# Performance work log

Measured on AMD Instinct MI355X. Metric: run time of the kernel, lower is better.

The kernel has to match this reference:

```python
import jax, jax.numpy as jnp
import numpy as np

B, N, M, D = 32, 1024, 256, 512
NEG_INF = -1e9  # keras Softmax mask additive constant


def _length_mask(key, batch, length):
    # realistic padding masks: first L positions valid, L >= length//4
    lens = jax.random.randint(key, (batch,), length // 4, length + 1)
    return jnp.arange(length)[None, :] < lens[:, None]


def setup_inputs() -> dict:
    key = jax.random.key(0)
    k1, k2, k3, k4, k5 = jax.random.split(key, 5)
    context = jax.random.normal(k1, (B, N, D), dtype=jnp.float32)
    query = jax.random.normal(k2, (B, M, D), dtype=jnp.float32)
    c_mask = _length_mask(k3, B, N)
    q_mask = _length_mask(k4, B, M)
    # Dense(units=1, use_bias=False) kernel over concat([q, c, q*c]) -> (3D, 1)
    w = jax.random.normal(k5, (3 * D, 1), dtype=jnp.float32) * (1.0 / np.sqrt(3 * D))
    return {"context": context, "query": query, "c_mask": c_mask, "q_mask": q_mask, "w": w}


def reference(context, query, c_mask, q_mask, w):
    d = context.shape[-1]
    # stack order in original: [q_matrix, c_matrix, q*c]
    w_q = w[:d, 0]
    w_c = w[d:2 * d, 0]
    w_m = w[2 * d:, 0]
    # trilinear similarity S[b,n,m] = q_j.w_q + c_i.w_c + (c_i*q_j).w_m, decomposed
    S = (context @ w_c)[:, :, None] \
        + (query @ w_q)[:, None, :] \
        + jnp.einsum('bnd,bmd->bnm', context * w_m, query)
    # context-direction softmax over query axis (axis=2), masked by q_mask
    A = jax.nn.softmax(jnp.where(q_mask[:, None, :], S, NEG_INF), axis=2)
    # query-direction softmax over context axis (axis=1), masked by c_mask
    Bm = jax.nn.softmax(jnp.where(c_mask[:, :, None], S, NEG_INF), axis=1)
    # context-to-query attention: A @ query -> (b, n, d)
    c2q = jnp.einsum('bnm,bmd->bnd', A, query)
    # query-to-context: (A @ B^T) @ context -> (b, n, d)
    q2c = jnp.einsum('bnk,bjk,bjd->bnd', A, Bm, context)
    out = jnp.concatenate([context, c2q, context * c2q, context * q2c], axis=-1)
    return out
```

## Files before the change

### kernel.cpp

```cpp
#include <hip/hip_runtime.h>
#include <hip/hip_bf16.h>

#define B_ 32
#define N_ 1024
#define M_ 256
#define D_ 512

typedef __attribute__((ext_vector_type(8))) short short8;
typedef __attribute__((ext_vector_type(4))) float f32x4;

#define OFF_S     ((size_t)0)
#define OFF_CTXW  ((size_t)8388608)
#define OFF_ANM   ((size_t)8388608)
#define OFF_BMT   ((size_t)12582912)
#define OFF_QB    ((size_t)16777216)
#define OFF_QT    ((size_t)18874368)
#define OFF_CT    ((size_t)20971520)
#define OFF_CDOT  ((size_t)29360128)
#define OFF_QDOT  ((size_t)29392896)
#define OFF_RMAX  ((size_t)29401088)
#define OFF_RSUM  ((size_t)29433856)
#define OFF_CMAX  ((size_t)29466624)
#define OFF_CSUM  ((size_t)29474816)
#define OFF_PMAX  ((size_t)29483008)
#define OFF_PSUM  ((size_t)29614080)


__global__ __launch_bounds__(256) void prep_ctxw(
    const float* __restrict__ ctx, const float* __restrict__ w,
    __hip_bfloat16* __restrict__ ctxw)
{
    size_t i4 = ((size_t)blockIdx.x * 256 + threadIdx.x) * 4;
    int d = (int)(i4 & (D_ - 1));
    float4 c = *(const float4*)(ctx + i4);
    float4 wm = *(const float4*)(w + 2 * D_ + d);
    __hip_bfloat16 o[4] __attribute__((aligned(8)));
    o[0] = __float2bfloat16(c.x * wm.x);
    o[1] = __float2bfloat16(c.y * wm.y);
    o[2] = __float2bfloat16(c.z * wm.z);
    o[3] = __float2bfloat16(c.w * wm.w);
    *(ushort4*)(ctxw + i4) = *(ushort4*)o;
}

__global__ __launch_bounds__(256) void prep_qry(
    const float* __restrict__ qry, __hip_bfloat16* __restrict__ qb)
{
    size_t i4 = ((size_t)blockIdx.x * 256 + threadIdx.x) * 4;
    float4 c = *(const float4*)(qry + i4);
    __hip_bfloat16 o[4] __attribute__((aligned(8)));
    o[0] = __float2bfloat16(c.x);
    o[1] = __float2bfloat16(c.y);
    o[2] = __float2bfloat16(c.z);
    o[3] = __float2bfloat16(c.w);
    *(ushort4*)(qb + i4) = *(ushort4*)o;
}

__global__ __launch_bounds__(256) void transpose_cast(
    const float* __restrict__ src, __hip_bfloat16* __restrict__ dst,
    int rows, int cols)
{
    __shared__ float t[64][65];
    int b = blockIdx.z, r0 = blockIdx.y * 64, c0 = blockIdx.x * 64;
    int tr = threadIdx.x >> 6, tc = threadIdx.x & 63;
    const float* sp = src + ((size_t)b * rows + r0) * cols + c0;
#pragma unroll
    for (int i = 0; i < 16; ++i)
        t[tr + i * 4][tc] = sp[(size_t)(tr + i * 4) * cols + tc];
    __syncthreads();
    __hip_bfloat16* dp = dst + ((size_t)b * cols + c0) * rows + r0;
#pragma unroll
    for (int i = 0; i < 16; ++i)
        dp[(size_t)(tr + i * 4) * rows + tc] = __float2bfloat16(t[tc][tr + i * 4]);
}

__global__ __launch_bounds__(256) void dots_kernel(
    const float* __restrict__ ctx, const float* __restrict__ qry,
    const float* __restrict__ w, float* __restrict__ cdot, float* __restrict__ qdot)
{
    int row  = blockIdx.x * 4 + (threadIdx.x >> 6);
    int lane = threadIdx.x & 63;
    const float* src; const float* wp; float* dst;
    if (row < B_ * N_) {
        src = ctx + (size_t)row * D_; wp = w + D_;
        dst = cdot + row;
    } else {
        int rr = row - B_ * N_;
        src = qry + (size_t)rr * D_; wp = w;
        dst = qdot + rr;
    }
    float s = 0.f;
#pragma unroll
    for (int i = 0; i < D_ / 64; ++i)
        s = fmaf(src[lane + 64 * i], wp[lane + 64 * i], s);
#pragma unroll
    for (int off = 32; off; off >>= 1) s += __shfl_down(s, off, 64);
    if (lane == 0) *dst = s;
}


__device__ __forceinline__ void gl2lds16(const __hip_bfloat16* g, __hip_bfloat16* l) {
    __builtin_amdgcn_global_load_lds(
        (const __attribute__((address_space(1))) unsigned int*)g,
        (__attribute__((address_space(3))) unsigned int*)l, 16, 0, 0);
}

template<int KTOT>
__device__ __forceinline__ void mfma128(
    const __hip_bfloat16* __restrict__ Abase, int lda,
    const __hip_bfloat16* __restrict__ Bbase, int ldb,
    __hip_bfloat16* As, __hip_bfloat16* Bs, f32x4 acc[4][4])
{
    const int tid = threadIdx.x;
    const int w = tid >> 6, lane = tid & 63;
    const int quad = lane >> 4, lr = lane & 15;
    const int wr = w >> 1, wc = w & 1;
    const int srow = w * 32 + (lane >> 2);
    const int scol = (lane & 3) * 8;
    const __hip_bfloat16* ga0 = Abase + (size_t)srow * lda + scol;
    const __hip_bfloat16* ga1 = ga0 + (size_t)16 * lda;
    const __hip_bfloat16* gb0 = Bbase + (size_t)srow * ldb + scol;
    const __hip_bfloat16* gb1 = gb0 + (size_t)16 * ldb;
    __hip_bfloat16* la0 = As + w * 1024;
    __hip_bfloat16* la1 = As + w * 1024 + 512;
    __hip_bfloat16* lb0 = Bs + w * 1024;
    __hip_bfloat16* lb1 = Bs + w * 1024 + 512;
    const int aoff = (wr * 64 + lr) * 32 + quad * 8;
    const int boff = (wc * 64 + lr) * 32 + quad * 8;

    for (int k0 = 0; k0 < KTOT; k0 += 32) {
        gl2lds16(ga0, la0); gl2lds16(ga1, la1);
        gl2lds16(gb0, lb0); gl2lds16(gb1, lb1);
        ga0 += 32; ga1 += 32; gb0 += 32; gb1 += 32;
        asm volatile("s_waitcnt vmcnt(0)" ::: "memory");
        __syncthreads();
        short8 a[4], bb[4];
        const short8* ap = (const short8*)(As + aoff);
        const short8* bp = (const short8*)(Bs + boff);
#pragma unroll
        for (int fi = 0; fi < 4; ++fi) a[fi] = ap[fi * 64];
#pragma unroll
        for (int fj = 0; fj < 4; ++fj) bb[fj] = bp[fj * 64];
#pragma unroll
        for (int fi = 0; fi < 4; ++fi)
#pragma unroll
            for (int fj = 0; fj < 4; ++fj)
                acc[fi][fj] = __builtin_amdgcn_mfma_f32_16x16x32_bf16(
                    a[fi], bb[fj], acc[fi][fj], 0, 0, 0);
        __syncthreads();
    }
}

#define ACC_INIT f32x4 acc[4][4]; \
    _Pragma("unroll") for (int i = 0; i < 4; ++i) \
    _Pragma("unroll") for (int j = 0; j < 4; ++j) acc[i][j] = (f32x4){0.f, 0.f, 0.f, 0.f};

#define EPI_IDX const int tid = threadIdx.x, lane = tid & 63, quad = lane >> 4, lr = lane & 15; \
    const int wr = tid >> 7, wc = (tid >> 6) & 1;

__global__ __launch_bounds__(256) void s_gemm_mfma(
    const __hip_bfloat16* __restrict__ ctxw, const __hip_bfloat16* __restrict__ qryb,
    const float* __restrict__ cdot, const float* __restrict__ qdot,
    float* __restrict__ S)
{
    __shared__ __align__(16) __hip_bfloat16 As[4096], Bs[4096];
    const int b = blockIdx.z, n0 = blockIdx.y * 128, m0 = blockIdx.x * 128;
    ACC_INIT
    mfma128<512>(ctxw + ((size_t)b * N_ + n0) * D_, D_,
                 qryb + ((size_t)b * M_ + m0) * D_, D_, As, Bs, acc);
    EPI_IDX
#pragma unroll
    for (int fi = 0; fi < 4; ++fi) {
#pragma unroll
        for (int r = 0; r < 4; ++r) {
            int n = n0 + wr * 64 + fi * 16 + quad * 4 + r;
            float cd = cdot[b * N_ + n];
            size_t rowoff = ((size_t)b * N_ + n) * M_;
#pragma unroll
            for (int fj = 0; fj < 4; ++fj) {
                int m = m0 + wc * 64 + fj * 16 + lr;
                S[rowoff + m] = acc[fi][fj][r] + cd + qdot[b * M_ + m];
            }
        }
    }
}

__global__ __launch_bounds__(256) void q2cpart_mfma(
    const __hip_bfloat16* __restrict__ ctxT, const __hip_bfloat16* __restrict__ BmT,
    __hip_bfloat16* __restrict__ Q2CT)
{
    __shared__ __align__(16) __hip_bfloat16 As[4096], Bs[4096];
    const int b = blockIdx.z, d0 = blockIdx.y * 128, m0 = blockIdx.x * 128;
    ACC_INIT
    mfma128<1024>(ctxT + ((size_t)b * D_ + d0) * N_, N_,
                  BmT + ((size_t)b * M_ + m0) * N_, N_, As, Bs, acc);
    EPI_IDX
#pragma unroll
    for (int fi = 0; fi < 4; ++fi) {
#pragma unroll
        for (int r = 0; r < 4; ++r) {
            int d = d0 + wr * 64 + fi * 16 + quad * 4 + r;
#pragma unroll
            for (int fj = 0; fj < 4; ++fj) {
                int m = m0 + wc * 64 + fj * 16 + lr;
                Q2CT[((size_t)b * D_ + d) * M_ + m] = __float2bfloat16(acc[fi][fj][r]);
            }
        }
    }
}

__global__ __launch_bounds__(256) void c2q_mfma(
    const __hip_bfloat16* __restrict__ Anm, const __hip_bfloat16* __restrict__ qryT,
    const float* __restrict__ ctx, float* __restrict__ out)
{
    __shared__ __align__(16) __hip_bfloat16 As[4096], Bs[4096];
    const int b = blockIdx.z, n0 = blockIdx.y * 128, d0 = blockIdx.x * 128;
    ACC_INIT
    mfma128<256>(Anm + ((size_t)b * N_ + n0) * M_, M_,
                 qryT + ((size_t)b * D_ + d0) * M_, M_, As, Bs, acc);
    EPI_IDX
#pragma unroll
    for (int fi = 0; fi < 4; ++fi) {
#pragma unroll
        for (int r = 0; r < 4; ++r) {
            int n = n0 + wr * 64 + fi * 16 + quad * 4 + r;
            size_t ibase = ((size_t)b * N_ + n) * D_;
            size_t obase = ((size_t)b * N_ + n) * (4 * D_);
#pragma unroll
            for (int fj = 0; fj < 4; ++fj) {
                int d = d0 + wc * 64 + fj * 16 + lr;
                float c = ctx[ibase + d];
                float v = acc[fi][fj][r];
                out[obase + d] = c;
                out[obase + D_ + d] = v;
                out[obase + 2 * D_ + d] = c * v;
            }
        }
    }
}

__global__ __launch_bounds__(256) void q2c_mfma(
    const __hip_bfloat16* __restrict__ Anm, const __hip_bfloat16* __restrict__ Q2CT,
    const float* __restrict__ ctx, float* __restrict__ out)
{
    __shared__ __align__(16) __hip_bfloat16 As[4096], Bs[4096];
    const int b = blockIdx.z, n0 = blockIdx.y * 128, d0 = blockIdx.x * 128;
    ACC_INIT
    mfma128<256>(Anm + ((size_t)b * N_ + n0) * M_, M_,
                 Q2CT + ((size_t)b * D_ + d0) * M_, M_, As, Bs, acc);
    EPI_IDX
#pragma unroll
    for (int fi = 0; fi < 4; ++fi) {
#pragma unroll
        for (int r = 0; r < 4; ++r) {
            int n = n0 + wr * 64 + fi * 16 + quad * 4 + r;
            size_t ibase = ((size_t)b * N_ + n) * D_;
            size_t obase = ((size_t)b * N_ + n) * (4 * D_);
#pragma unroll
            for (int fj = 0; fj < 4; ++fj) {
                int d = d0 + wc * 64 + fj * 16 + lr;
                out[obase + 3 * D_ + d] = ctx[ibase + d] * acc[fi][fj][r];
            }
        }
    }
}


__global__ __launch_bounds__(256) void row_stats(
    const float* __restrict__ S, const int* __restrict__ q_mask,
    float* __restrict__ rmax, float* __restrict__ rsum)
{
    int row  = blockIdx.x * 4 + (threadIdx.x >> 6);
    int lane = threadIdx.x & 63;
    int b = row >> 10;
    const float* Sp = S + (size_t)row * M_;
    const int* qm = q_mask + b * M_;
    float v[4];
    float mx = -1e30f;
#pragma unroll
    for (int i = 0; i < 4; ++i) {
        int m = lane + 64 * i;
        float x = qm[m] ? Sp[m] : -1e9f;
        v[i] = x; mx = fmaxf(mx, x);
    }
#pragma unroll
    for (int off = 32; off; off >>= 1) mx = fmaxf(mx, __shfl_down(mx, off, 64));
    mx = __shfl(mx, 0, 64);
    float sm = 0.f;
#pragma unroll
    for (int i = 0; i < 4; ++i) sm += __expf(v[i] - mx);
#pragma unroll
    for (int off = 32; off; off >>= 1) sm += __shfl_down(sm, off, 64);
    if (lane == 0) { rmax[row] = mx; rsum[row] = sm; }
}

__global__ __launch_bounds__(256) void col_stats_part(
    const float* __restrict__ S, const int* __restrict__ c_mask,
    float* __restrict__ pmax, float* __restrict__ psum)
{
    int b = blockIdx.y, ch = blockIdx.x, m = threadIdx.x;
    const float* Sp = S + ((size_t)b * N_ + ch * 64) * M_;
    const int* cm = c_mask + b * N_ + ch * 64;
    float mx = -1e30f, sm = 0.f;
    for (int n = 0; n < 64; ++n) {
        float x = cm[n] ? Sp[(size_t)n * M_ + m] : -1e9f;
        if (x > mx) { sm = sm * __expf(mx - x) + 1.f; mx = x; }
        else        { sm += __expf(x - mx); }
    }
    pmax[((size_t)b * 16 + ch) * M_ + m] = mx;
    psum[((size_t)b * 16 + ch) * M_ + m] = sm;
}

__global__ __launch_bounds__(256) void col_stats_combine(
    const float* __restrict__ pmax, const float* __restrict__ psum,
    float* __restrict__ cmax, float* __restrict__ csum)
{
    int idx = blockIdx.x * 256 + threadIdx.x;
    int b = idx >> 8, m = idx & 255;
    float mx = -1e30f;
#pragma unroll
    for (int ch = 0; ch < 16; ++ch)
        mx = fmaxf(mx, pmax[((size_t)b * 16 + ch) * M_ + m]);
    float sm = 0.f;
#pragma unroll
    for (int ch = 0; ch < 16; ++ch)
        sm += psum[((size_t)b * 16 + ch) * M_ + m] *
              __expf(pmax[((size_t)b * 16 + ch) * M_ + m] - mx);
    cmax[idx] = mx; csum[idx] = sm;
}

__global__ __launch_bounds__(256) void normalize_kernel(
    const float* __restrict__ S, __hip_bfloat16* __restrict__ Anm,
    __hip_bfloat16* __restrict__ BmT,
    const int* __restrict__ q_mask, const int* __restrict__ c_mask,
    const float* __restrict__ rmax, const float* __restrict__ rsum,
    const float* __restrict__ cmax, const float* __restrict__ csum)
{
    __shared__ float t[64][65];
    int b = blockIdx.z, n0 = blockIdx.y * 64, m0 = blockIdx.x * 64;
    int tr = threadIdx.x >> 6, tc = threadIdx.x & 63;
    int m = m0 + tc;
    int qm = q_mask[b * M_ + m];
    float cmx = cmax[b * M_ + m], csm = csum[b * M_ + m];
#pragma unroll
    for (int i = 0; i < 16; ++i) {
        int n = n0 + tr + i * 4;
        size_t idx = ((size_t)b * N_ + n) * M_ + m;
        float s = S[idx];
        float a  = qm ? __expf(s - rmax[b * N_ + n]) / rsum[b * N_ + n] : 0.f;
        float bm = c_mask[b * N_ + n] ? __expf(s - cmx) / csm : 0.f;
        Anm[idx] = __float2bfloat16(a);
        t[tc][tr + i * 4] = bm;
    }
    __syncthreads();
#pragma unroll
    for (int i = 0; i < 16; ++i) {
        int ml = tr + i * 4;
        BmT[((size_t)b * M_ + m0 + ml) * N_ + n0 + tc] = __float2bfloat16(t[ml][tc]);
    }
}

extern "C" void kernel_launch(void* const* d_in, const int* in_sizes, int n_in,
                              void* d_out, int out_size, void* d_ws, size_t ws_size,
                              hipStream_t stream) {
    const float* ctx   = (const float*)d_in[0];
    const float* qry   = (const float*)d_in[1];
    const int*   cmask = (const int*)d_in[2];
    const int*   qmask = (const int*)d_in[3];
    const float* w     = (const float*)d_in[4];
    float* out = (float*)d_out;
    float* ws  = (float*)d_ws;

    float* S = ws + OFF_S;
    __hip_bfloat16* ctxw = (__hip_bfloat16*)(ws + OFF_CTXW);
    __hip_bfloat16* Anm  = (__hip_bfloat16*)(ws + OFF_ANM);
    __hip_bfloat16* BmT  = (__hip_bfloat16*)(ws + OFF_BMT);
    __hip_bfloat16* qb   = (__hip_bfloat16*)(ws + OFF_QB);
    __hip_bfloat16* Q2CT = (__hip_bfloat16*)(ws + OFF_QB);
    __hip_bfloat16* qT   = (__hip_bfloat16*)(ws + OFF_QT);
    __hip_bfloat16* cT   = (__hip_bfloat16*)(ws + OFF_CT);
    float* cdot = ws + OFF_CDOT;
    float* qdot = ws + OFF_QDOT;
    float* rmax = ws + OFF_RMAX;
    float* rsum = ws + OFF_RSUM;
    float* cmx  = ws + OFF_CMAX;
    float* csm  = ws + OFF_CSUM;
    float* pmax = ws + OFF_PMAX;
    float* psum = ws + OFF_PSUM;

    prep_ctxw<<<B_ * N_ * D_ / 1024, 256, 0, stream>>>(ctx, w, ctxw);
    prep_qry<<<B_ * M_ * D_ / 1024, 256, 0, stream>>>(qry, qb);
    dim3 gtc(D_ / 64, N_ / 64, B_);
    transpose_cast<<<gtc, 256, 0, stream>>>(ctx, cT, N_, D_);
    dim3 gtq(D_ / 64, M_ / 64, B_);
    transpose_cast<<<gtq, 256, 0, stream>>>(qry, qT, M_, D_);
    dots_kernel<<<(B_ * N_ + B_ * M_) / 4, 256, 0, stream>>>(ctx, qry, w, cdot, qdot);

    dim3 gS(M_ / 128, N_ / 128, B_);
    s_gemm_mfma<<<gS, 256, 0, stream>>>(ctxw, qb, cdot, qdot, S);

    row_stats<<<B_ * N_ / 4, 256, 0, stream>>>(S, qmask, rmax, rsum);
    dim3 gC(16, B_);
    col_stats_part<<<gC, 256, 0, stream>>>(S, cmask, pmax, psum);
    col_stats_combine<<<B_ * M_ / 256, 256, 0, stream>>>(pmax, psum, cmx, csm);

    dim3 gN(M_ / 64, N_ / 64, B_);
    normalize_kernel<<<gN, 256, 0, stream>>>(S, Anm, BmT, qmask, cmask,
                                             rmax, rsum, cmx, csm);

    dim3 gP(M_ / 128, D_ / 128, B_);
    q2cpart_mfma<<<gP, 256, 0, stream>>>(cT, BmT, Q2CT);

    dim3 gO(D_ / 128, N_ / 128, B_);
    c2q_mfma<<<gO, 256, 0, stream>>>(Anm, qT, ctx, out);
    q2c_mfma<<<gO, 256, 0, stream>>>(Anm, Q2CT, ctx, out);
}
```

Measured before the change: 534.6 us.

## Fuse prep, softmax stats into S GEMM epilogue, and merge output GEMMs

Merges the cast, transpose and dot-product prep kernels into one pass per input, with atomics accumulating the dot products into a zeroed buffer. Computes per-tile row and column softmax partial max/sum inside the S GEMM epilogue, so row_stats and col_stats_part no longer re-read S, and a single kernel combines the partials. Fuses the c2q and q2c GEMMs into one kernel that shares the A tile loads and writes all four output slices. The cost is more launch-free atomics, higher register and LDS pressure in the fused kernels, and a small extra memset.

```diff
diff --git a/kernel.cpp b/kernel.cpp
--- a/kernel.cpp
+++ b/kernel.cpp
@@ -24,77 +24,66 @@
 #define OFF_CSUM  ((size_t)29474816)
 #define OFF_PMAX  ((size_t)29483008)
 #define OFF_PSUM  ((size_t)29614080)
-
-
-__global__ __launch_bounds__(256) void prep_ctxw(
+#define OFF_RPMAX ((size_t)29745152)
+#define OFF_RPSUM ((size_t)29876224)
+
+__global__ __launch_bounds__(256) void prep_ctx(
     const float* __restrict__ ctx, const float* __restrict__ w,
-    __hip_bfloat16* __restrict__ ctxw)
-{
-    size_t i4 = ((size_t)blockIdx.x * 256 + threadIdx.x) * 4;
-    int d = (int)(i4 & (D_ - 1));
-    float4 c = *(const float4*)(ctx + i4);
-    float4 wm = *(const float4*)(w + 2 * D_ + d);
-    __hip_bfloat16 o[4] __attribute__((aligned(8)));
-    o[0] = __float2bfloat16(c.x * wm.x);
-    o[1] = __float2bfloat16(c.y * wm.y);
-    o[2] = __float2bfloat16(c.z * wm.z);
-    o[3] = __float2bfloat16(c.w * wm.w);
-    *(ushort4*)(ctxw + i4) = *(ushort4*)o;
-}
-
-__global__ __launch_bounds__(256) void prep_qry(
-    const float* __restrict__ qry, __hip_bfloat16* __restrict__ qb)
-{
-    size_t i4 = ((size_t)blockIdx.x * 256 + threadIdx.x) * 4;
-    float4 c = *(const float4*)(qry + i4);
-    __hip_bfloat16 o[4] __attribute__((aligned(8)));
-    o[0] = __float2bfloat16(c.x);
-    o[1] = __float2bfloat16(c.y);
-    o[2] = __float2bfloat16(c.z);
-    o[3] = __float2bfloat16(c.w);
-    *(ushort4*)(qb + i4) = *(ushort4*)o;
-}
-
-__global__ __launch_bounds__(256) void transpose_cast(
-    const float* __restrict__ src, __hip_bfloat16* __restrict__ dst,
-    int rows, int cols)
+    __hip_bfloat16* __restrict__ ctxw, __hip_bfloat16* __restrict__ cT,
+    float* __restrict__ cdot)
 {
     __shared__ float t[64][65];
-    int b = blockIdx.z, r0 = blockIdx.y * 64, c0 = blockIdx.x * 64;
+    int b = blockIdx.z, n0 = blockIdx.y * 64, d0 = blockIdx.x * 64;
     int tr = threadIdx.x >> 6, tc = threadIdx.x & 63;
-    const float* sp = src + ((size_t)b * rows + r0) * cols + c0;
+    const float* sp = ctx + ((size_t)b * N_ + n0) * D_ + d0;
+    __hip_bfloat16* cwp = ctxw + ((size_t)b * N_ + n0) * D_ + d0;
+    float wmv = w[2 * D_ + d0 + tc];
+    float wcv = w[D_ + d0 + tc];
+#pragma unroll
+    for (int i = 0; i < 16; ++i) {
+        int r = tr + i * 4;
+        float x = sp[(size_t)r * D_ + tc];
+        t[r][tc] = x;
+        cwp[(size_t)r * D_ + tc] = __float2bfloat16(x * wmv);
+        float p = x * wcv;
+#pragma unroll
+        for (int off = 32; off; off >>= 1) p += __shfl_down(p, off, 64);
+        if (tc == 0) atomicAdd(cdot + b * N_ + n0 + r, p);
+    }
+    __syncthreads();
+    __hip_bfloat16* dp = cT + ((size_t)b * D_ + d0) * N_ + n0;
 #pragma unroll
     for (int i = 0; i < 16; ++i)
-        t[tr + i * 4][tc] = sp[(size_t)(tr + i * 4) * cols + tc];
+        dp[(size_t)(tr + i * 4) * N_ + tc] = __float2bfloat16(t[tc][tr + i * 4]);
+}
+
+__global__ __launch_bounds__(256) void prep_q(
+    const float* __restrict__ qry, const float* __restrict__ w,
+    __hip_bfloat16* __restrict__ qb, __hip_bfloat16* __restrict__ qT,
+    float* __restrict__ qdot)
+{
+    __shared__ float t[64][65];
+    int b = blockIdx.z, m0 = blockIdx.y * 64, d0 = blockIdx.x * 64;
+    int tr = threadIdx.x >> 6, tc = threadIdx.x & 63;
+    const float* sp = qry + ((size_t)b * M_ + m0) * D_ + d0;
+    __hip_bfloat16* qbp = qb + ((size_t)b * M_ + m0) * D_ + d0;
+    float wqv = w[d0 + tc];
+#pragma unroll
+    for (int i = 0; i < 16; ++i) {
+        int r = tr + i * 4;
+        float x = sp[(size_t)r * D_ + tc];
+        t[r][tc] = x;
+        qbp[(size_t)r * D_ + tc] = __float2bfloat16(x);
+        float p = x * wqv;
+#pragma unroll
+        for (int off = 32; off; off >>= 1) p += __shfl_down(p, off, 64);
+        if (tc == 0) atomicAdd(qdot + b * M_ + m0 + r, p);
+    }
     __syncthreads();
-    __hip_bfloat16* dp = dst + ((size_t)b * cols + c0) * rows + r0;
+    __hip_bfloat16* dp = qT + ((size_t)b * D_ + d0) * M_ + m0;
 #pragma unroll
     for (int i = 0; i < 16; ++i)
-        dp[(size_t)(tr + i * 4) * rows + tc] = __float2bfloat16(t[tc][tr + i * 4]);
-}
-
-__global__ __launch_bounds__(256) void dots_kernel(
-    const float* __restrict__ ctx, const float* __restrict__ qry,
-    const float* __restrict__ w, float* __restrict__ cdot, float* __restrict__ qdot)
-{
-    int row  = blockIdx.x * 4 + (threadIdx.x >> 6);
-    int lane = threadIdx.x & 63;
-    const float* src; const float* wp; float* dst;
-    if (row < B_ * N_) {
-        src = ctx + (size_t)row * D_; wp = w + D_;
-        dst = cdot + row;
-    } else {
-        int rr = row - B_ * N_;
-        src = qry + (size_t)rr * D_; wp = w;
-        dst = qdot + rr;
-    }
-    float s = 0.f;
-#pragma unroll
-    for (int i = 0; i < D_ / 64; ++i)
-        s = fmaf(src[lane + 64 * i], wp[lane + 64 * i], s);
-#pragma unroll
-    for (int off = 32; off; off >>= 1) s += __shfl_down(s, off, 64);
-    if (lane == 0) *dst = s;
+        dp[(size_t)(tr + i * 4) * M_ + tc] = __float2bfloat16(t[tc][tr + i * 4]);
 }
 
 
@@ -150,36 +139,166 @@
     }
 }
 
-#define ACC_INIT f32x4 acc[4][4]; \
-    _Pragma("unroll") for (int i = 0; i < 4; ++i) \
-    _Pragma("unroll") for (int j = 0; j < 4; ++j) acc[i][j] = (f32x4){0.f, 0.f, 0.f, 0.f};
+template<int KTOT>
+__device__ __forceinline__ void mfma128x2(
+    const __hip_bfloat16* __restrict__ Abase, int lda,
+    const __hip_bfloat16* __restrict__ B1base,
+    const __hip_bfloat16* __restrict__ B2base, int ldb,
+    __hip_bfloat16* As, __hip_bfloat16* B1s, __hip_bfloat16* B2s,
+    f32x4 acc1[4][4], f32x4 acc2[4][4])
+{
+    const int tid = threadIdx.x;
+    const int w = tid >> 6, lane = tid & 63;
+    const int quad = lane >> 4, lr = lane & 15;
+    const int wr = w >> 1, wc = w & 1;
+    const int srow = w * 32 + (lane >> 2);
+    const int scol = (lane & 3) * 8;
+    const __hip_bfloat16* ga0 = Abase + (size_t)srow * lda + scol;
+    const __hip_bfloat16* ga1 = ga0 + (size_t)16 * lda;
+    const __hip_bfloat16* gb10 = B1base + (size_t)srow * ldb + scol;
+    const __hip_bfloat16* gb11 = gb10 + (size_t)16 * ldb;
+    const __hip_bfloat16* gb20 = B2base + (size_t)srow * ldb + scol;
+    const __hip_bfloat16* gb21 = gb20 + (size_t)16 * ldb;
+    __hip_bfloat16* la0 = As + w * 1024;
+    __hip_bfloat16* la1 = la0 + 512;
+    __hip_bfloat16* lb10 = B1s + w * 1024;
+    __hip_bfloat16* lb11 = lb10 + 512;
+    __hip_bfloat16* lb20 = B2s + w * 1024;
+    __hip_bfloat16* lb21 = lb20 + 512;
+    const int aoff = (wr * 64 + lr) * 32 + quad * 8;
+    const int boff = (wc * 64 + lr) * 32 + quad * 8;
+
+    for (int k0 = 0; k0 < KTOT; k0 += 32) {
+        gl2lds16(ga0, la0); gl2lds16(ga1, la1);
+        gl2lds16(gb10, lb10); gl2lds16(gb11, lb11);
+        gl2lds16(gb20, lb20); gl2lds16(gb21, lb21);
+        ga0 += 32; ga1 += 32; gb10 += 32; gb11 += 32; gb20 += 32; gb21 += 32;
+        asm volatile("s_waitcnt vmcnt(0)" ::: "memory");
+        __syncthreads();
+        short8 a[4], b1[4], b2[4];
+        const short8* ap = (const short8*)(As + aoff);
+        const short8* bp1 = (const short8*)(B1s + boff);
+        const short8* bp2 = (const short8*)(B2s + boff);
+#pragma unroll
+        for (int fi = 0; fi < 4; ++fi) a[fi] = ap[fi * 64];
+#pragma unroll
+        for (int fj = 0; fj < 4; ++fj) { b1[fj] = bp1[fj * 64]; b2[fj] = bp2[fj * 64]; }
+#pragma unroll
+        for (int fi = 0; fi < 4; ++fi)
+#pragma unroll
+            for (int fj = 0; fj < 4; ++fj) {
+                acc1[fi][fj] = __builtin_amdgcn_mfma_f32_16x16x32_bf16(
+                    a[fi], b1[fj], acc1[fi][fj], 0, 0, 0);
+                acc2[fi][fj] = __builtin_amdgcn_mfma_f32_16x16x32_bf16(
+                    a[fi], b2[fj], acc2[fi][fj], 0, 0, 0);
+            }
+        __syncthreads();
+    }
+}
+
+#define ACC_INIT(acc) \
+    _Pragma("unroll") for (int i_ = 0; i_ < 4; ++i_) \
+    _Pragma("unroll") for (int j_ = 0; j_ < 4; ++j_) acc[i_][j_] = (f32x4){0.f, 0.f, 0.f, 0.f};
 
 #define EPI_IDX const int tid = threadIdx.x, lane = tid & 63, quad = lane >> 4, lr = lane & 15; \
     const int wr = tid >> 7, wc = (tid >> 6) & 1;
 
-__global__ __launch_bounds__(256) void s_gemm_mfma(
+__global__ __launch_bounds__(256) void s_gemm_stats(
     const __hip_bfloat16* __restrict__ ctxw, const __hip_bfloat16* __restrict__ qryb,
     const float* __restrict__ cdot, const float* __restrict__ qdot,
-    float* __restrict__ S)
+    const int* __restrict__ q_mask, const int* __restrict__ c_mask,
+    float* __restrict__ S,
+    float* __restrict__ rpmax, float* __restrict__ rpsum,
+    float* __restrict__ pmax, float* __restrict__ psum)
 {
     __shared__ __align__(16) __hip_bfloat16 As[4096], Bs[4096];
     const int b = blockIdx.z, n0 = blockIdx.y * 128, m0 = blockIdx.x * 128;
-    ACC_INIT
+    f32x4 acc[4][4];
+    ACC_INIT(acc)
     mfma128<512>(ctxw + ((size_t)b * N_ + n0) * D_, D_,
                  qryb + ((size_t)b * M_ + m0) * D_, D_, As, Bs, acc);
     EPI_IDX
-#pragma unroll
-    for (int fi = 0; fi < 4; ++fi) {
+    float cd[4][4]; int cmv[4][4];
+#pragma unroll
+    for (int fi = 0; fi < 4; ++fi)
 #pragma unroll
         for (int r = 0; r < 4; ++r) {
             int n = n0 + wr * 64 + fi * 16 + quad * 4 + r;
-            float cd = cdot[b * N_ + n];
+            cd[fi][r] = cdot[b * N_ + n];
+            cmv[fi][r] = c_mask[b * N_ + n];
+        }
+    float qd[4]; int qmv[4];
+#pragma unroll
+    for (int fj = 0; fj < 4; ++fj) {
+        int m = m0 + wc * 64 + fj * 16 + lr;
+        qd[fj] = qdot[b * M_ + m];
+        qmv[fj] = q_mask[b * M_ + m];
+    }
+#pragma unroll
+    for (int fi = 0; fi < 4; ++fi)
+#pragma unroll
+        for (int r = 0; r < 4; ++r) {
+            int n = n0 + wr * 64 + fi * 16 + quad * 4 + r;
             size_t rowoff = ((size_t)b * N_ + n) * M_;
 #pragma unroll
             for (int fj = 0; fj < 4; ++fj) {
                 int m = m0 + wc * 64 + fj * 16 + lr;
-                S[rowoff + m] = acc[fi][fj][r] + cd + qdot[b * M_ + m];
-            }
+                S[rowoff + m] = acc[fi][fj][r] + cd[fi][r] + qd[fj];
+            }
+        }
+    const int part = blockIdx.x * 2 + wc;
+#pragma unroll
+    for (int fi = 0; fi < 4; ++fi)
+#pragma unroll
+        for (int r = 0; r < 4; ++r) {
+            float xs[4], mx = -1e30f;
+#pragma unroll
+            for (int fj = 0; fj < 4; ++fj) {
+                xs[fj] = qmv[fj] ? (acc[fi][fj][r] + cd[fi][r] + qd[fj]) : -1e9f;
+                mx = fmaxf(mx, xs[fj]);
+            }
+#pragma unroll
+            for (int off = 1; off < 16; off <<= 1)
+                mx = fmaxf(mx, __shfl_xor(mx, off, 64));
+            float se = 0.f;
+#pragma unroll
+            for (int fj = 0; fj < 4; ++fj) se += __expf(xs[fj] - mx);
+#pragma unroll
+            for (int off = 1; off < 16; off <<= 1)
+                se += __shfl_xor(se, off, 64);
+            if (lr == 0) {
+                int n = n0 + wr * 64 + fi * 16 + quad * 4 + r;
+                rpmax[((size_t)b * N_ + n) * 4 + part] = mx;
+                rpsum[((size_t)b * N_ + n) * 4 + part] = se;
+            }
+        }
+    const int ch = blockIdx.y * 2 + wr;
+#pragma unroll
+    for (int fj = 0; fj < 4; ++fj) {
+        float mx = -1e30f;
+#pragma unroll
+        for (int fi = 0; fi < 4; ++fi)
+#pragma unroll
+            for (int r = 0; r < 4; ++r) {
+                float x = cmv[fi][r] ? (acc[fi][fj][r] + cd[fi][r] + qd[fj]) : -1e9f;
+                mx = fmaxf(mx, x);
+            }
+        mx = fmaxf(mx, __shfl_xor(mx, 16, 64));
+        mx = fmaxf(mx, __shfl_xor(mx, 32, 64));
+        float se = 0.f;
+#pragma unroll
+        for (int fi = 0; fi < 4; ++fi)
+#pragma unroll
+            for (int r = 0; r < 4; ++r) {
+                float x = cmv[fi][r] ? (acc[fi][fj][r] + cd[fi][r] + qd[fj]) : -1e9f;
+                se += __expf(x - mx);
+            }
+        se += __shfl_xor(se, 16, 64);
+        se += __shfl_xor(se, 32, 64);
+        if (lane < 16) {
+            int m = m0 + wc * 64 + fj * 16 + lr;
+            pmax[((size_t)b * 16 + ch) * M_ + m] = mx;
+            psum[((size_t)b * 16 + ch) * M_ + m] = se;
         }
     }
 }
@@ -190,7 +309,8 @@
 {
     __shared__ __align__(16) __hip_bfloat16 As[4096], Bs[4096];
     const int b = blockIdx.z, d0 = blockIdx.y * 128, m0 = blockIdx.x * 128;
-    ACC_INIT
+    f32x4 acc[4][4];
+    ACC_INIT(acc)
     mfma128<1024>(ctxT + ((size_t)b * D_ + d0) * N_, N_,
                   BmT + ((size_t)b * M_ + m0) * N_, N_, As, Bs, acc);
     EPI_IDX
@@ -208,15 +328,20 @@
     }
 }
 
-__global__ __launch_bounds__(256) void c2q_mfma(
+__global__ __launch_bounds__(256) void out_fused_mfma(
     const __hip_bfloat16* __restrict__ Anm, const __hip_bfloat16* __restrict__ qryT,
-    const float* __restrict__ ctx, float* __restrict__ out)
-{
-    __shared__ __align__(16) __hip_bfloat16 As[4096], Bs[4096];
+    const __hip_bfloat16* __restrict__ Q2CT, const float* __restrict__ ctx,
+    float* __restrict__ out)
+{
+    __shared__ __align__(16) __hip_bfloat16 As[4096], B1s[4096], B2s[4096];
     const int b = blockIdx.z, n0 = blockIdx.y * 128, d0 = blockIdx.x * 128;
-    ACC_INIT
-    mfma128<256>(Anm + ((size_t)b * N_ + n0) * M_, M_,
-                 qryT + ((size_t)b * D_ + d0) * M_, M_, As, Bs, acc);
+    f32x4 acc1[4][4], acc2[4][4];
+    ACC_INIT(acc1)
+    ACC_INIT(acc2)
+    mfma128x2<256>(Anm + ((size_t)b * N_ + n0) * M_, M_,
+                   qryT + ((size_t)b * D_ + d0) * M_,
+                   Q2CT + ((size_t)b * D_ + d0) * M_, M_,
+                   As, B1s, B2s, acc1, acc2);
     EPI_IDX
 #pragma unroll
     for (int fi = 0; fi < 4; ++fi) {
@@ -229,103 +354,50 @@
             for (int fj = 0; fj < 4; ++fj) {
                 int d = d0 + wc * 64 + fj * 16 + lr;
                 float c = ctx[ibase + d];
-                float v = acc[fi][fj][r];
+                float v1 = acc1[fi][fj][r];
+                float v2 = acc2[fi][fj][r];
                 out[obase + d] = c;
-                out[obase + D_ + d] = v;
-                out[obase + 2 * D_ + d] = c * v;
-            }
-        }
-    }
-}
-
-__global__ __launch_bounds__(256) void q2c_mfma(
-    const __hip_bfloat16* __restrict__ Anm, const __hip_bfloat16* __restrict__ Q2CT,
-    const float* __restrict__ ctx, float* __restrict__ out)
-{
-    __shared__ __align__(16) __hip_bfloat16 As[4096], Bs[4096];
-    const int b = blockIdx.z, n0 = blockIdx.y * 128, d0 = blockIdx.x * 128;
-    ACC_INIT
-    mfma128<256>(Anm + ((size_t)b * N_ + n0) * M_, M_,
-                 Q2CT + ((size_t)b * D_ + d0) * M_, M_, As, Bs, acc);
-    EPI_IDX
-#pragma unroll
-    for (int fi = 0; fi < 4; ++fi) {
-#pragma unroll
-        for (int r = 0; r < 4; ++r) {
-            int n = n0 + wr * 64 + fi * 16 + quad * 4 + r;
-            size_t ibase = ((size_t)b * N_ + n) * D_;
-            size_t obase = ((size_t)b * N_ + n) * (4 * D_);
-#pragma unroll
-            for (int fj = 0; fj < 4; ++fj) {
-                int d = d0 + wc * 64 + fj * 16 + lr;
-                out[obase + 3 * D_ + d] = ctx[ibase + d] * acc[fi][fj][r];
-            }
-        }
-    }
-}
-
-
-__global__ __launch_bounds__(256) void row_stats(
-    const float* __restrict__ S, const int* __restrict__ q_mask,
+                out[obase + D_ + d] = v1;
+                out[obase + 2 * D_ + d] = c * v1;
+                out[obase + 3 * D_ + d] = c * v2;
+            }
+        }
+    }
+}
+
+
+__global__ __launch_bounds__(256) void combine_stats(
+    const float* __restrict__ pmax, const float* __restrict__ psum,
+    const float* __restrict__ rpmax, const float* __restrict__ rpsum,
+    float* __restrict__ cmax, float* __restrict__ csum,
     float* __restrict__ rmax, float* __restrict__ rsum)
 {
-    int row  = blockIdx.x * 4 + (threadIdx.x >> 6);
-    int lane = threadIdx.x & 63;
-    int b = row >> 10;
-    const float* Sp = S + (size_t)row * M_;
-    const int* qm = q_mask + b * M_;
-    float v[4];
-    float mx = -1e30f;
-#pragma unroll
-    for (int i = 0; i < 4; ++i) {
-        int m = lane + 64 * i;
-        float x = qm[m] ? Sp[m] : -1e9f;
-        v[i] = x; mx = fmaxf(mx, x);
-    }
-#pragma unroll
-    for (int off = 32; off; off >>= 1) mx = fmaxf(mx, __shfl_down(mx, off, 64));
-    mx = __shfl(mx, 0, 64);
-    float sm = 0.f;
-#pragma unroll
-    for (int i = 0; i < 4; ++i) sm += __expf(v[i] - mx);
-#pragma unroll
-    for (int off = 32; off; off >>= 1) sm += __shfl_down(sm, off, 64);
-    if (lane == 0) { rmax[row] = mx; rsum[row] = sm; }
-}
-
-__global__ __launch_bounds__(256) void col_stats_part(
-    const float* __restrict__ S, const int* __restrict__ c_mask,
-    float* __restrict__ pmax, float* __restrict__ psum)
-{
-    int b = blockIdx.y, ch = blockIdx.x, m = threadIdx.x;
-    const float* Sp = S + ((size_t)b * N_ + ch * 64) * M_;
-    const int* cm = c_mask + b * N_ + ch * 64;
-    float mx = -1e30f, sm = 0.f;
-    for (int n = 0; n < 64; ++n) {
-        float x = cm[n] ? Sp[(size_t)n * M_ + m] : -1e9f;
-        if (x > mx) { sm = sm * __expf(mx - x) + 1.f; mx = x; }
-        else        { sm += __expf(x - mx); }
-    }
-    pmax[((size_t)b * 16 + ch) * M_ + m] = mx;
-    psum[((size_t)b * 16 + ch) * M_ + m] = sm;
-}
-
-__global__ __launch_bounds__(256) void col_stats_combine(
-    const float* __restrict__ pmax, const float* __restrict__ psum,
-    float* __restrict__ cmax, float* __restrict__ csum)
-{
     int idx = blockIdx.x * 256 + threadIdx.x;
-    int b = idx >> 8, m = idx & 255;
-    float mx = -1e30f;
-#pragma unroll
-    for (int ch = 0; ch < 16; ++ch)
-        mx = fmaxf(mx, pmax[((size_t)b * 16 + ch) * M_ + m]);
-    float sm = 0.f;
-#pragma unroll
-    for (int ch = 0; ch < 16; ++ch)
-        sm += psum[((size_t)b * 16 + ch) * M_ + m] *
-              __expf(pmax[((size_t)b * 16 + ch) * M_ + m] - mx);
-    cmax[idx] = mx; csum[idx] = sm;
+    if (idx < B_ * M_) {
+        int b = idx >> 8, m = idx & 255;
+        float mx = -1e30f;
+#pragma unroll
+        for (int ch = 0; ch < 16; ++ch)
+            mx = fmaxf(mx, pmax[((size_t)b * 16 + ch) * M_ + m]);
+        float sm = 0.f;
+#pragma unroll
+        for (int ch = 0; ch < 16; ++ch)
+            sm += psum[((size_t)b * 16 + ch) * M_ + m] *
+                  __expf(pmax[((size_t)b * 16 + ch) * M_ + m] - mx);
+        cmax[idx] = mx; csum[idx] = sm;
+    } else {
+        int row = idx - B_ * M_;
+        float mx = -1e30f;
+#pragma unroll
+        for (int p = 0; p < 4; ++p)
+            mx = fmaxf(mx, rpmax[(size_t)row * 4 + p]);
+        float sm = 0.f;
+#pragma unroll
+        for (int p = 0; p < 4; ++p)
+            sm += rpsum[(size_t)row * 4 + p] *
+                  __expf(rpmax[(size_t)row * 4 + p] - mx);
+        rmax[row] = mx; rsum[row] = sm;
+    }
 }
 
 __global__ __launch_bounds__(256) void normalize_kernel(
@@ -386,22 +458,22 @@
     float* csm  = ws + OFF_CSUM;
     float* pmax = ws + OFF_PMAX;
     float* psum = ws + OFF_PSUM;
-
-    prep_ctxw<<<B_ * N_ * D_ / 1024, 256, 0, stream>>>(ctx, w, ctxw);
-    prep_qry<<<B_ * M_ * D_ / 1024, 256, 0, stream>>>(qry, qb);
-    dim3 gtc(D_ / 64, N_ / 64, B_);
-    transpose_cast<<<gtc, 256, 0, stream>>>(ctx, cT, N_, D_);
-    dim3 gtq(D_ / 64, M_ / 64, B_);
-    transpose_cast<<<gtq, 256, 0, stream>>>(qry, qT, M_, D_);
-    dots_kernel<<<(B_ * N_ + B_ * M_) / 4, 256, 0, stream>>>(ctx, qry, w, cdot, qdot);
+    float* rpmax = ws + OFF_RPMAX;
+    float* rpsum = ws + OFF_RPSUM;
+
+    hipMemsetAsync(cdot, 0, (size_t)(B_ * N_ + B_ * M_) * sizeof(float), stream);
+
+    dim3 gpc(D_ / 64, N_ / 64, B_);
+    prep_ctx<<<gpc, 256, 0, stream>>>(ctx, w, ctxw, cT, cdot);
+    dim3 gpq(D_ / 64, M_ / 64, B_);
+    prep_q<<<gpq, 256, 0, stream>>>(qry, w, qb, qT, qdot);
 
     dim3 gS(M_ / 128, N_ / 128, B_);
-    s_gemm_mfma<<<gS, 256, 0, stream>>>(ctxw, qb, cdot, qdot, S);
-
-    row_stats<<<B_ * N_ / 4, 256, 0, stream>>>(S, qmask, rmax, rsum);
-    dim3 gC(16, B_);
-    col_stats_part<<<gC, 256, 0, stream>>>(S, cmask, pmax, psum);
-    col_stats_combine<<<B_ * M_ / 256, 256, 0, stream>>>(pmax, psum, cmx, csm);
+    s_gemm_stats<<<gS, 256, 0, stream>>>(ctxw, qb, cdot, qdot, qmask, cmask,
+                                         S, rpmax, rpsum, pmax, psum);
+
+    combine_stats<<<(B_ * M_ + B_ * N_) / 256, 256, 0, stream>>>(
+        pmax, psum, rpmax, rpsum, cmx, csm, rmax, rsum);
 
     dim3 gN(M_ / 64, N_ / 64, B_);
     normalize_kernel<<<gN, 256, 0, stream>>>(S, Anm, BmT, qmask, cmask,
@@ -411,6 +483,5 @@
     q2cpart_mfma<<<gP, 256, 0, stream>>>(cT, BmT, Q2CT);
 
     dim3 gO(D_ / 128, N_ / 128, B_);
-    c2q_mfma<<<gO, 256, 0, stream>>>(Anm, qT, ctx, out);
-    q2c_mfma<<<gO, 256, 0, stream>>>(Anm, Q2CT, ctx, out);
-}
+    out_fused_mfma<<<gO, 256, 0, stream>>>(Anm, qT, Q2CT, ctx, out);
+}
```

Result: faster. 504.8 us (-5.6%).
